# Kernel tuning notes

Measured on AMD Instinct MI355X. Metric: run time of the kernel, lower is better.

The kernel has to match this reference:

```python
import jax, jax.numpy as jnp
import numpy as np

N_NODES = 100000
EPS = 1e-5


def gcn_conv(x, src, dst, W, b):
    # PyG GCNConv: h = W x; out_i = sum_{j->i} norm_ij * h_j  (with self-loops)
    h = x @ W  # [N, out]
    deg = jax.ops.segment_sum(jnp.ones_like(src, dtype=h.dtype), dst,
                              num_segments=N_NODES) + 1.0  # +1 self-loop
    dinv = jax.lax.rsqrt(deg)  # [N]
    norm = dinv[src] * dinv[dst]  # [E]
    msgs = h[src] * norm[:, None]  # [E, out]
    agg = jax.ops.segment_sum(msgs, dst, num_segments=N_NODES)
    agg = agg + h * (1.0 / deg)[:, None]  # self-loop term, norm = deg^-1
    return agg + b


def graph_norm(x, w, b, mean_scale):
    # PyG GraphNorm, single graph: normalize over nodes per feature
    mean = jnp.mean(x, axis=0, keepdims=True)
    xc = x - mean_scale * mean
    var = jnp.mean(xc * xc, axis=0, keepdims=True)
    return w * xc * jax.lax.rsqrt(var + EPS) + b


def layer_norm(x, w, b):
    mean = jnp.mean(x, axis=-1, keepdims=True)
    xc = x - mean
    var = jnp.mean(xc * xc, axis=-1, keepdims=True)
    return w * xc * jax.lax.rsqrt(var + EPS) + b


def setup_inputs() -> dict:
    key = jax.random.key(0)
    ks = jax.random.split(key, 8)
    in_dim, hid, emb = 128, 64, 32
    x = jax.random.normal(ks[0], (N_NODES, in_dim), dtype=jnp.float32)
    edge_index = jax.random.randint(ks[1], (2, 1600000), 0, N_NODES, dtype=jnp.int64)
    s = 0.05
    return {
        'x': x,
        'edge_index': edge_index,
        'W1': jax.random.normal(ks[2], (in_dim, hid), jnp.float32) * s,
        'b1': jnp.zeros((hid,), jnp.float32),
        'W2': jax.random.normal(ks[3], (hid, hid), jnp.float32) * s,
        'b2': jnp.zeros((hid,), jnp.float32),
        'gn_w': jnp.ones((hid,), jnp.float32),
        'gn_b': jnp.zeros((hid,), jnp.float32),
        'gn_ms': jnp.ones((hid,), jnp.float32),
        'ln_w': jnp.ones((hid,), jnp.float32),
        'ln_b': jnp.zeros((hid,), jnp.float32),
        'fc_W': jax.random.normal(ks[4], (hid, emb), jnp.float32) * s,
        'fc_b': jnp.zeros((emb,), jnp.float32),
    }


def reference(x, edge_index, W1, b1, W2, b2, gn_w, gn_b, gn_ms, ln_w, ln_b, fc_W, fc_b):
    src, dst = edge_index[0], edge_index[1]
    h = jax.nn.relu(gcn_conv(x, src, dst, W1, b1))
    h = graph_norm(h, gn_w, gn_b, gn_ms)
    h = layer_norm(h, ln_w, ln_b)
    # dropout: identity in eval mode
    h = jax.nn.relu(gcn_conv(h, src, dst, W2, b2))
    h = graph_norm(h, gn_w, gn_b, gn_ms)
    h = layer_norm(h, ln_w, ln_b)
    pooled = jnp.max(h, axis=0)  # [hid]
    embedding = pooled @ fc_W + fc_b  # [emb]; emb != 1 so no sigmoid
    return embedding
```

## Files before the change

### kernel.cpp

```cpp
#include <hip/hip_runtime.h>
#include <hip/hip_bf16.h>

#define EPSV 1e-5f
#define CHUNK 256
#define CAP 6144
#define MAXNB 512
#define EPB 4096

typedef __attribute__((ext_vector_type(8))) short bf16x8;
typedef __attribute__((ext_vector_type(4))) float f32x4;

__device__ __forceinline__ ushort f2bf(float f) {
    union { float f; unsigned u; } c; c.f = f;
    unsigned u = c.u;
    return (ushort)((u + 0x7fffu + ((u >> 16) & 1u)) >> 16);
}
__device__ __forceinline__ float bf2f(ushort h) {
    union { unsigned u; float f; } c; c.u = ((unsigned)h) << 16;
    return c.f;
}
__device__ __forceinline__ float bflo(unsigned u) {
    union { unsigned u; float f; } c; c.u = u << 16;
    return c.f;
}
__device__ __forceinline__ float bfhi(unsigned u) {
    union { unsigned u; float f; } c; c.u = u & 0xFFFF0000u;
    return c.f;
}
__device__ __forceinline__ void acc8(float* a, uint4 u) {
    a[0] += bflo(u.x); a[1] += bfhi(u.x);
    a[2] += bflo(u.y); a[3] += bfhi(u.y);
    a[4] += bflo(u.z); a[5] += bfhi(u.z);
    a[6] += bflo(u.w); a[7] += bfhi(u.w);
}


__global__ void prep_kernel(const float* __restrict__ W1, const float* __restrict__ W2,
                            ushort* __restrict__ wsw1, ushort* __restrict__ wsw2,
                            uint4* __restrict__ zr, int nz16) {
    int t = blockIdx.x * blockDim.x + threadIdx.x;
    if (t < 128 * 64) {
        int k = t >> 6, n = t & 63;
        wsw1[((k >> 3) * 64 + n) * 8 + (k & 7)] = f2bf(W1[t]);
    }
    if (t < 64 * 64) {
        int k = t >> 6, n = t & 63;
        wsw2[((k >> 3) * 64 + n) * 8 + (k & 7)] = f2bf(W2[t]);
    }
    if (t < nz16) zr[t] = make_uint4(0u, 0u, 0u, 0u);
}


__global__ void __launch_bounds__(256) bucket_scatter(const int* __restrict__ ei,
                                                      int* __restrict__ bcur,
                                                      unsigned* __restrict__ bdata, int E,
                                                      int NB) {
    __shared__ int h[MAXNB];
    __shared__ int cur[MAXNB];
    int t = threadIdx.x;
    int base = blockIdx.x * EPB;
    int end = min(base + EPB, E);
    for (int b = t; b < NB; b += 256) h[b] = 0;
    __syncthreads();
    for (int e = base + t * 4; e < end; e += 1024) {
        int4 d4 = *reinterpret_cast<const int4*>(&ei[E + e]);
        atomicAdd(&h[d4.x >> 8], 1);
        atomicAdd(&h[d4.y >> 8], 1);
        atomicAdd(&h[d4.z >> 8], 1);
        atomicAdd(&h[d4.w >> 8], 1);
    }
    __syncthreads();
    for (int b = t; b < NB; b += 256) {
        int c = h[b];
        cur[b] = c ? (atomicAdd(&bcur[b], c) + b * CAP) : 0;
    }
    __syncthreads();
    for (int e = base + t * 4; e < end; e += 1024) {
        int4 s4 = *reinterpret_cast<const int4*>(&ei[e]);
        int4 d4 = *reinterpret_cast<const int4*>(&ei[E + e]);
        int p0 = atomicAdd(&cur[d4.x >> 8], 1);
        bdata[p0] = (unsigned)s4.x | ((unsigned)(d4.x & 255) << 20);
        int p1 = atomicAdd(&cur[d4.y >> 8], 1);
        bdata[p1] = (unsigned)s4.y | ((unsigned)(d4.y & 255) << 20);
        int p2 = atomicAdd(&cur[d4.z >> 8], 1);
        bdata[p2] = (unsigned)s4.z | ((unsigned)(d4.z & 255) << 20);
        int p3 = atomicAdd(&cur[d4.w >> 8], 1);
        bdata[p3] = (unsigned)s4.w | ((unsigned)(d4.w & 255) << 20);
    }
}


__global__ void __launch_bounds__(256) bucket_finish(const unsigned* __restrict__ bdata,
                                                     const int* __restrict__ bcur,
                                                     int2* __restrict__ NI,
                                                     float* __restrict__ dinv,
                                                     int* __restrict__ srcs, int N) {
    __shared__ int h[CHUNK];
    __shared__ int cur[CHUNK];
    int t = threadIdx.x;
    int beg = blockIdx.x * CAP;
    int end = beg + bcur[blockIdx.x];
    h[t] = 0;
    __syncthreads();
    for (int e = beg + t; e < end; e += 256) atomicAdd(&h[bdata[e] >> 20], 1);
    __syncthreads();
    int deg = h[t];
    int pc = (deg + 3) & ~3;
    cur[t] = pc;
    __syncthreads();
    for (int off = 1; off < 256; off <<= 1) {
        int x = (t >= off) ? cur[t - off] : 0;
        __syncthreads();
        cur[t] += x;
        __syncthreads();
    }
    int begp = beg + cur[t] - pc;
    int node = blockIdx.x * CHUNK + t;
    if (node < N) {
        NI[node] = make_int2(begp, pc);
        dinv[node] = rsqrtf((float)deg + 1.0f);
    }
    h[t] = begp;
    __syncthreads();
    for (int e = beg + t; e < end; e += 256) {
        unsigned p = bdata[e];
        int pos = atomicAdd(&h[p >> 20], 1);
        srcs[pos] = (int)((p & 0xFFFFFu) << 3);
    }
    __syncthreads();
    int zr = N * 8;
    for (int k = h[t]; k < begp + pc; k++) srcs[k] = zr;
}


__global__ void __launch_bounds__(256) mm1_kernel(const float* __restrict__ X,
                                                  const ushort* __restrict__ wsw,
                                                  const float* __restrict__ dinv,
                                                  ushort* __restrict__ Ht, int N) {
    const int KO = 4;
    int w = threadIdx.x >> 6, lane = threadIdx.x & 63;
    int m = lane & 15, q = lane >> 4;
    int row = blockIdx.x * 64 + w * 16 + m;

    bf16x8 afrag[KO];
#pragma unroll
    for (int kk = 0; kk < KO; kk++) {
        float xv[8];
        if (row < N) {
            const float4* xp = reinterpret_cast<const float4*>(X + (size_t)row * 128 + kk * 32 + q * 8);
            float4 v0 = xp[0], v1 = xp[1];
            xv[0] = v0.x; xv[1] = v0.y; xv[2] = v0.z; xv[3] = v0.w;
            xv[4] = v1.x; xv[5] = v1.y; xv[6] = v1.z; xv[7] = v1.w;
        } else {
#pragma unroll
            for (int j = 0; j < 8; j++) xv[j] = 0.f;
        }
#pragma unroll
        for (int j = 0; j < 8; j++) afrag[kk][j] = (short)f2bf(xv[j]);
    }

    float dv[4];
#pragma unroll
    for (int reg = 0; reg < 4; reg++) {
        int r = blockIdx.x * 64 + w * 16 + q * 4 + reg;
        dv[reg] = (r < N) ? dinv[r] : 0.f;
    }

    const bf16x8* wp = reinterpret_cast<const bf16x8*>(wsw);
#pragma unroll
    for (int ct = 0; ct < 4; ct++) {
        f32x4 acc = {0.f, 0.f, 0.f, 0.f};
#pragma unroll
        for (int kk = 0; kk < KO; kk++) {
            bf16x8 b = wp[(kk * 4 + q) * 64 + ct * 16 + m];
            acc = __builtin_amdgcn_mfma_f32_16x16x32_bf16(afrag[kk], b, acc, 0, 0, 0);
        }
#pragma unroll
        for (int reg = 0; reg < 4; reg++) {
            int r = blockIdx.x * 64 + w * 16 + q * 4 + reg;
            if (r < N) Ht[(size_t)r * 64 + ct * 16 + m] = f2bf(acc[reg] * dv[reg]);
        }
    }
}


__global__ void __launch_bounds__(256) mm2_kernel(
    const ushort* __restrict__ A2, const ushort* __restrict__ wsw,
    const float* __restrict__ sums, const float* __restrict__ gn_w,
    const float* __restrict__ gn_b, const float* __restrict__ gn_ms,
    const float* __restrict__ ln_w, const float* __restrict__ ln_b,
    const float* __restrict__ dinv, ushort* __restrict__ Ht, int N) {
    __shared__ float sg[64], tg[64], lwv[64], lbv[64];
    int t = threadIdx.x;
    if (t < 64) {
        float invN = 1.0f / (float)N;
        float mean = sums[t] * invN;
        float m2 = sums[64 + t] * invN;
        float ms = gn_ms[t];
        float var = m2 - 2.f * ms * mean * mean + ms * ms * mean * mean;
        float s = gn_w[t] * rsqrtf(var + EPSV);
        sg[t] = s;
        tg[t] = gn_b[t] - s * ms * mean;
        lwv[t] = ln_w[t];
        lbv[t] = ln_b[t];
    }
    __syncthreads();

    int w = t >> 6, lane = t & 63;
    int m = lane & 15, q = lane >> 4;
    int row = blockIdx.x * 64 + w * 16 + m;

    float g[16];
#pragma unroll
    for (int kk = 0; kk < 2; kk++) {
        uint4 u = make_uint4(0, 0, 0, 0);
        if (row < N)
            u = *reinterpret_cast<const uint4*>(A2 + (size_t)row * 64 + kk * 32 + q * 8);
        unsigned uu[4] = {u.x, u.y, u.z, u.w};
#pragma unroll
        for (int p = 0; p < 4; p++) {
            int f0 = kk * 32 + q * 8 + 2 * p;
            g[kk * 8 + 2 * p] = sg[f0] * bflo(uu[p]) + tg[f0];
            g[kk * 8 + 2 * p + 1] = sg[f0 + 1] * bfhi(uu[p]) + tg[f0 + 1];
        }
    }
    float s1 = 0.f;
#pragma unroll
    for (int i = 0; i < 16; i++) s1 += g[i];
    s1 += __shfl_xor(s1, 16);
    s1 += __shfl_xor(s1, 32);
    float mu = s1 * (1.f / 64.f);
    float s2 = 0.f;
#pragma unroll
    for (int i = 0; i < 16; i++) {
        float c = g[i] - mu;
        s2 += c * c;
    }
    s2 += __shfl_xor(s2, 16);
    s2 += __shfl_xor(s2, 32);
    float rs = rsqrtf(s2 * (1.f / 64.f) + EPSV);

    bf16x8 afrag[2];
#pragma unroll
    for (int kk = 0; kk < 2; kk++) {
#pragma unroll
        for (int j = 0; j < 8; j++) {
            int f = kk * 32 + q * 8 + j;
            float y = lwv[f] * (g[kk * 8 + j] - mu) * rs + lbv[f];
            afrag[kk][j] = (short)f2bf(y);
        }
    }

    float dv[4];
#pragma unroll
    for (int reg = 0; reg < 4; reg++) {
        int r = blockIdx.x * 64 + w * 16 + q * 4 + reg;
        dv[reg] = (r < N) ? dinv[r] : 0.f;
    }

    const bf16x8* wp = reinterpret_cast<const bf16x8*>(wsw);
#pragma unroll
    for (int ct = 0; ct < 4; ct++) {
        f32x4 acc = {0.f, 0.f, 0.f, 0.f};
#pragma unroll
        for (int kk = 0; kk < 2; kk++) {
            bf16x8 b = wp[(kk * 4 + q) * 64 + ct * 16 + m];
            acc = __builtin_amdgcn_mfma_f32_16x16x32_bf16(afrag[kk], b, acc, 0, 0, 0);
        }
#pragma unroll
        for (int reg = 0; reg < 4; reg++) {
            int r = blockIdx.x * 64 + w * 16 + q * 4 + reg;
            if (r < N) Ht[(size_t)r * 64 + ct * 16 + m] = f2bf(acc[reg] * dv[reg]);
        }
    }
}


__global__ void __launch_bounds__(256) agg_kernel(
    const ushort* __restrict__ Ht, const int2* __restrict__ NI, const int* __restrict__ srcs,
    const float* __restrict__ dinv, const float* __restrict__ bias,
    ushort* __restrict__ out, float* __restrict__ sums, int N) {
    int t = threadIdx.x;
    int lane = t & 63;
    int g = lane >> 3, fq = lane & 7;
    int wid = (blockIdx.x * blockDim.x + t) >> 6;
    int nw = (gridDim.x * blockDim.x) >> 6;
    const uint4* H4 = reinterpret_cast<const uint4*>(Ht);
    uint4* O4 = reinterpret_cast<uint4*>(out);
    const int ZR = N * 8;
    float bb[8];
#pragma unroll
    for (int j = 0; j < 8; j++) bb[j] = bias[fq * 8 + j];
    float ps1[8] = {0, 0, 0, 0, 0, 0, 0, 0}, ps2[8] = {0, 0, 0, 0, 0, 0, 0, 0};

    for (int jo = wid; jo * 8 < N; jo += nw) {
        int node = jo * 8 + g;
        bool valid = node < N;
        int2 info = valid ? NI[node] : make_int2(0, 0);
        float di = valid ? dinv[node] : 0.f;
        int e = info.x, end = info.x + info.y;
        float a[8] = {0, 0, 0, 0, 0, 0, 0, 0};
        for (; e + 8 <= end; e += 8) {
            int4 i0 = *reinterpret_cast<const int4*>(&srcs[e]);
            int4 i1 = *reinterpret_cast<const int4*>(&srcs[e + 4]);
            uint4 u0 = H4[i0.x + fq];
            uint4 u1 = H4[i0.y + fq];
            uint4 u2 = H4[i0.z + fq];
            uint4 u3 = H4[i0.w + fq];
            uint4 u4 = H4[i1.x + fq];
            uint4 u5 = H4[i1.y + fq];
            uint4 u6 = H4[i1.z + fq];
            uint4 u7 = H4[i1.w + fq];
            acc8(a, u0); acc8(a, u1); acc8(a, u2); acc8(a, u3);
            acc8(a, u4); acc8(a, u5); acc8(a, u6); acc8(a, u7);
        }
        if (e < end) {
            int4 i0 = *reinterpret_cast<const int4*>(&srcs[e]);
            uint4 u0 = H4[i0.x + fq];
            uint4 u1 = H4[i0.y + fq];
            uint4 u2 = H4[i0.z + fq];
            uint4 u3 = H4[i0.w + fq];
            acc8(a, u0); acc8(a, u1); acc8(a, u2); acc8(a, u3);
        }
        uint4 us = H4[(valid ? node * 8 : ZR) + fq];
        float sf[8] = {bflo(us.x), bfhi(us.x), bflo(us.y), bfhi(us.y),
                       bflo(us.z), bfhi(us.z), bflo(us.w), bfhi(us.w)};
        float vv[8];
#pragma unroll
        for (int j = 0; j < 8; j++) vv[j] = fmaxf(di * a[j] + di * sf[j] + bb[j], 0.f);
        if (valid) {
            uint4 o;
            o.x = (unsigned)f2bf(vv[0]) | ((unsigned)f2bf(vv[1]) << 16);
            o.y = (unsigned)f2bf(vv[2]) | ((unsigned)f2bf(vv[3]) << 16);
            o.z = (unsigned)f2bf(vv[4]) | ((unsigned)f2bf(vv[5]) << 16);
            o.w = (unsigned)f2bf(vv[6]) | ((unsigned)f2bf(vv[7]) << 16);
            O4[(size_t)node * 8 + fq] = o;
#pragma unroll
            for (int j = 0; j < 8; j++) {
                ps1[j] += vv[j];
                ps2[j] += vv[j] * vv[j];
            }
        }
    }

    __shared__ float red[4][128];
    int wv = t >> 6;
#pragma unroll
    for (int j = 0; j < 8; j++) {
        float s = ps1[j], q = ps2[j];
        s += __shfl_xor(s, 8); s += __shfl_xor(s, 16); s += __shfl_xor(s, 32);
        q += __shfl_xor(q, 8); q += __shfl_xor(q, 16); q += __shfl_xor(q, 32);
        if (g == 0) {
            red[wv][fq * 8 + j] = s;
            red[wv][64 + fq * 8 + j] = q;
        }
    }
    __syncthreads();
    if (t < 128) {
        float v = red[0][t] + red[1][t] + red[2][t] + red[3][t];
        atomicAdd(&sums[t], v);
    }
}


__device__ __forceinline__ unsigned fkey(float f) {
    unsigned u = __float_as_uint(f);
    return (u & 0x80000000u) ? ~u : (u | 0x80000000u);
}

__global__ void __launch_bounds__(256) gnlnmax_final(
    const ushort* __restrict__ A, const float* __restrict__ sums,
    const float* __restrict__ gn_w, const float* __restrict__ gn_b,
    const float* __restrict__ gn_ms, const float* __restrict__ ln_w,
    const float* __restrict__ ln_b, unsigned* __restrict__ pooled,
    unsigned* __restrict__ done, const float* __restrict__ fc_W,
    const float* __restrict__ fc_b, float* __restrict__ out, int N) {
    __shared__ float sg[64], tg[64];
    int t = threadIdx.x;
    if (t < 64) {
        float invN = 1.0f / (float)N;
        float mean = sums[t] * invN;
        float m2 = sums[64 + t] * invN;
        float ms = gn_ms[t];
        float var = m2 - 2.f * ms * mean * mean + ms * ms * mean * mean;
        float s = gn_w[t] * rsqrtf(var + EPSV);
        sg[t] = s;
        tg[t] = gn_b[t] - s * ms * mean;
    }
    __syncthreads();

    int lane = t & 63;
    int g = lane >> 3, fq = lane & 7;
    float sgv[8], tgv[8], lwv[8], lbv[8];
#pragma unroll
    for (int j = 0; j < 8; j++) {
        sgv[j] = sg[fq * 8 + j];
        tgv[j] = tg[fq * 8 + j];
        lwv[j] = ln_w[fq * 8 + j];
        lbv[j] = ln_b[fq * 8 + j];
    }

    int wid = (blockIdx.x * blockDim.x + t) >> 6;
    int nw = (gridDim.x * blockDim.x) >> 6;
    const uint4* A4 = reinterpret_cast<const uint4*>(A);
    float mx[8];
#pragma unroll
    for (int j = 0; j < 8; j++) mx[j] = -3.4e38f;

    for (int jo = wid; jo * 8 < N; jo += nw) {
        int row = jo * 8 + g;
        bool valid = row < N;
        uint4 u = A4[(size_t)(valid ? row : 0) * 8 + fq];
        float y[8];
        y[0] = sgv[0] * bflo(u.x) + tgv[0];
        y[1] = sgv[1] * bfhi(u.x) + tgv[1];
        y[2] = sgv[2] * bflo(u.y) + tgv[2];
        y[3] = sgv[3] * bfhi(u.y) + tgv[3];
        y[4] = sgv[4] * bflo(u.z) + tgv[4];
        y[5] = sgv[5] * bfhi(u.z) + tgv[5];
        y[6] = sgv[6] * bflo(u.w) + tgv[6];
        y[7] = sgv[7] * bfhi(u.w) + tgv[7];
        float s1 = 0.f;
#pragma unroll
        for (int j = 0; j < 8; j++) s1 += y[j];
        s1 += __shfl_xor(s1, 1);
        s1 += __shfl_xor(s1, 2);
        s1 += __shfl_xor(s1, 4);
        float mu = s1 * (1.f / 64.f);
        float s2 = 0.f;
#pragma unroll
        for (int j = 0; j < 8; j++) {
            float c = y[j] - mu;
            s2 += c * c;
        }
        s2 += __shfl_xor(s2, 1);
        s2 += __shfl_xor(s2, 2);
        s2 += __shfl_xor(s2, 4);
        float rs = rsqrtf(s2 * (1.f / 64.f) + EPSV);
        if (valid) {
#pragma unroll
            for (int j = 0; j < 8; j++)
                mx[j] = fmaxf(mx[j], lwv[j] * (y[j] - mu) * rs + lbv[j]);
        }
    }

    __shared__ float red[4][64];
    int wv = t >> 6;
#pragma unroll
    for (int j = 0; j < 8; j++) {
        float m = mx[j];
        m = fmaxf(m, __shfl_xor(m, 8));
        m = fmaxf(m, __shfl_xor(m, 16));
        m = fmaxf(m, __shfl_xor(m, 32));
        if (g == 0) red[wv][fq * 8 + j] = m;
    }
    __syncthreads();
    if (t < 64) {
        float m = fmaxf(fmaxf(red[0][t], red[1][t]), fmaxf(red[2][t], red[3][t]));
        atomicMax(&pooled[t], fkey(m));
    }
    __syncthreads();
    __shared__ int islast;
    if (t == 0) {
        __threadfence();
        unsigned old = atomicAdd(done, 1u);
        islast = (old == gridDim.x - 1);
    }
    __syncthreads();
    if (islast) {
        __shared__ float p[64];
        if (t < 64) {
            __threadfence();
            unsigned u = atomicAdd(&pooled[t], 0u);
            p[t] = (u & 0x80000000u) ? __uint_as_float(u ^ 0x80000000u) : __uint_as_float(~u);
        }
        __syncthreads();
        if (t < 32) {
            float acc = fc_b[t];
#pragma unroll
            for (int f = 0; f < 64; f++) acc += p[f] * fc_W[f * 32 + t];
            out[t] = acc;
        }
    }
}


static inline size_t align_up(size_t v, size_t a) { return (v + a - 1) & ~(a - 1); }

extern "C" void kernel_launch(void* const* d_in, const int* in_sizes, int n_in, void* d_out,
                              int out_size, void* d_ws, size_t ws_size, hipStream_t stream) {
    const float* x = (const float*)d_in[0];
    const int* ei = (const int*)d_in[1];
    const float* W1 = (const float*)d_in[2];
    const float* b1 = (const float*)d_in[3];
    const float* W2 = (const float*)d_in[4];
    const float* b2 = (const float*)d_in[5];
    const float* gn_w = (const float*)d_in[6];
    const float* gn_b = (const float*)d_in[7];
    const float* gn_ms = (const float*)d_in[8];
    const float* ln_w = (const float*)d_in[9];
    const float* ln_b = (const float*)d_in[10];
    const float* fc_W = (const float*)d_in[11];
    const float* fc_b = (const float*)d_in[12];
    float* out = (float*)d_out;

    const int N = in_sizes[0] / 128;
    const int E = in_sizes[1] / 2;
    const int NB = (N + CHUNK - 1) / CHUNK;

    char* ws = (char*)d_ws;
    size_t off = 0;
    auto alloc = [&](size_t bytes) {
        char* p = ws + off;
        off = align_up(off + bytes, 256);
        return p;
    };
    int2* NI = (int2*)alloc((size_t)N * 8);
    float* dinv = (float*)alloc((size_t)N * 4);
    unsigned* bdata = (unsigned*)alloc((size_t)NB * CAP * 4);
    int* srcs = (int*)alloc((size_t)NB * CAP * 4);
    ushort* bufB = (ushort*)alloc((size_t)N * 64 * 2);
    ushort* wsw1 = (ushort*)alloc(128 * 64 * 2);
    ushort* wsw2 = (ushort*)alloc(64 * 64 * 2);
    ushort* bufA = (ushort*)alloc((size_t)N * 64 * 2);
    size_t zoff = off;
    ushort* zrow = (ushort*)alloc(128);
    float* sums = (float*)alloc(256 * 4);
    unsigned* pooled = (unsigned*)alloc(64 * 4);
    int* bcur = (int*)alloc((size_t)(NB + 1) * 4);
    unsigned* done = (unsigned*)alloc(4);
    size_t zlen = off - zoff;
    (void)zrow;

    int nbB = (E + EPB - 1) / EPB;
    prep_kernel<<<48, 256, 0, stream>>>(W1, W2, wsw1, wsw2, (uint4*)(ws + zoff),
                                        (int)(zlen / 16));
    bucket_scatter<<<nbB, 256, 0, stream>>>(ei, bcur, bdata, E, NB);
    bucket_finish<<<NB, 256, 0, stream>>>(bdata, bcur, NI, dinv, srcs, N);

    int nbMM = (N + 63) / 64;
    int nbAgg = 782;

    mm1_kernel<<<nbMM, 256, 0, stream>>>(x, wsw1, dinv, bufA, N);
    agg_kernel<<<nbAgg, 256, 0, stream>>>(bufA, NI, srcs, dinv, b1, bufB, sums, N);

    mm2_kernel<<<nbMM, 256, 0, stream>>>(bufB, wsw2, sums, gn_w, gn_b, gn_ms, ln_w, ln_b, dinv,
                                         bufA, N);
    agg_kernel<<<nbAgg, 256, 0, stream>>>(bufA, NI, srcs, dinv, b2, bufB, sums + 128, N);
    gnlnmax_final<<<512, 256, 0, stream>>>(bufB, sums + 128, gn_w, gn_b, gn_ms, ln_w, ln_b,
                                           pooled, done, fc_W, fc_b, out, N);
}
```

Before: 283.1 us.

## Quantize transformed node features to int8 with per-row scales for aggregation

The matmul kernels now write the dinv-scaled features as int8 with one float scale per row, in place of bf16. The aggregation kernel gathers 8-byte int8 groups plus a scale per neighbour and dequantizes while accumulating. This halves the bytes of the random gathers that dominate the edge aggregation, at the cost of an extra scale load per edge and reduced precision, which may exceed the reference tolerance.

```diff
diff --git a/kernel.cpp b/kernel.cpp
--- a/kernel.cpp
+++ b/kernel.cpp
@@ -27,17 +27,22 @@
     union { unsigned u; float f; } c; c.u = u & 0xFFFF0000u;
     return c.f;
 }
-__device__ __forceinline__ void acc8(float* a, uint4 u) {
-    a[0] += bflo(u.x); a[1] += bfhi(u.x);
-    a[2] += bflo(u.y); a[3] += bfhi(u.y);
-    a[4] += bflo(u.z); a[5] += bfhi(u.z);
-    a[6] += bflo(u.w); a[7] += bfhi(u.w);
+__device__ __forceinline__ void accq(float* a, uint2 g, float sc) {
+    a[0] += sc * (float)(signed char)(g.x & 0xFF);
+    a[1] += sc * (float)(signed char)((g.x >> 8) & 0xFF);
+    a[2] += sc * (float)(signed char)((g.x >> 16) & 0xFF);
+    a[3] += sc * (float)(signed char)(g.x >> 24);
+    a[4] += sc * (float)(signed char)(g.y & 0xFF);
+    a[5] += sc * (float)(signed char)((g.y >> 8) & 0xFF);
+    a[6] += sc * (float)(signed char)((g.y >> 16) & 0xFF);
+    a[7] += sc * (float)(signed char)(g.y >> 24);
 }
 
 
 __global__ void prep_kernel(const float* __restrict__ W1, const float* __restrict__ W2,
                             ushort* __restrict__ wsw1, ushort* __restrict__ wsw2,
-                            uint4* __restrict__ zr, int nz16) {
+                            uint4* __restrict__ zr, int nz16, char* __restrict__ T8,
+                            float* __restrict__ scales, int N) {
     int t = blockIdx.x * blockDim.x + threadIdx.x;
     if (t < 128 * 64) {
         int k = t >> 6, n = t & 63;
@@ -48,6 +53,8 @@
         wsw2[((k >> 3) * 64 + n) * 8 + (k & 7)] = f2bf(W2[t]);
     }
     if (t < nz16) zr[t] = make_uint4(0u, 0u, 0u, 0u);
+    if (t < 4) reinterpret_cast<uint4*>(T8 + (size_t)N * 64)[t] = make_uint4(0u, 0u, 0u, 0u);
+    if (t == 4) scales[N] = 0.f;
 }
 
 
@@ -133,14 +140,42 @@
 }
 
 
+__device__ __forceinline__ void quant_store(const f32x4* accs, const float* dv, int rbase,
+                                            int ml, char* __restrict__ T8,
+                                            float* __restrict__ scales, int N) {
+#pragma unroll
+    for (int reg = 0; reg < 4; reg++) {
+        float mx = fmaxf(fmaxf(fabsf(accs[0][reg]), fabsf(accs[1][reg])),
+                         fmaxf(fabsf(accs[2][reg]), fabsf(accs[3][reg])));
+        mx = fmaxf(mx, __shfl_xor(mx, 1));
+        mx = fmaxf(mx, __shfl_xor(mx, 2));
+        mx = fmaxf(mx, __shfl_xor(mx, 4));
+        mx = fmaxf(mx, __shfl_xor(mx, 8));
+        mx = fmaxf(mx * dv[reg], 1e-20f);
+        float inv = 127.f / mx;
+        int r = rbase + reg;
+        if (r < N) {
+            float s = dv[reg] * inv;
+#pragma unroll
+            for (int ct = 0; ct < 4; ct++) {
+                int qv = __float2int_rn(accs[ct][reg] * s);
+                T8[(size_t)r * 64 + ct * 16 + ml] = (char)qv;
+            }
+            if (ml == 0) scales[r] = mx * (1.f / 127.f);
+        }
+    }
+}
+
+
 __global__ void __launch_bounds__(256) mm1_kernel(const float* __restrict__ X,
                                                   const ushort* __restrict__ wsw,
                                                   const float* __restrict__ dinv,
-                                                  ushort* __restrict__ Ht, int N) {
+                                                  char* __restrict__ T8,
+                                                  float* __restrict__ scales, int N) {
     const int KO = 4;
     int w = threadIdx.x >> 6, lane = threadIdx.x & 63;
-    int m = lane & 15, q = lane >> 4;
-    int row = blockIdx.x * 64 + w * 16 + m;
+    int ml = lane & 15, q = lane >> 4;
+    int row = blockIdx.x * 64 + w * 16 + ml;
 
     bf16x8 afrag[KO];
 #pragma unroll
@@ -159,28 +194,27 @@
         for (int j = 0; j < 8; j++) afrag[kk][j] = (short)f2bf(xv[j]);
     }
 
+    int rbase = blockIdx.x * 64 + w * 16 + q * 4;
     float dv[4];
 #pragma unroll
     for (int reg = 0; reg < 4; reg++) {
-        int r = blockIdx.x * 64 + w * 16 + q * 4 + reg;
+        int r = rbase + reg;
         dv[reg] = (r < N) ? dinv[r] : 0.f;
     }
 
     const bf16x8* wp = reinterpret_cast<const bf16x8*>(wsw);
+    f32x4 accs[4];
 #pragma unroll
     for (int ct = 0; ct < 4; ct++) {
         f32x4 acc = {0.f, 0.f, 0.f, 0.f};
 #pragma unroll
         for (int kk = 0; kk < KO; kk++) {
-            bf16x8 b = wp[(kk * 4 + q) * 64 + ct * 16 + m];
+            bf16x8 b = wp[(kk * 4 + q) * 64 + ct * 16 + ml];
             acc = __builtin_amdgcn_mfma_f32_16x16x32_bf16(afrag[kk], b, acc, 0, 0, 0);
         }
-#pragma unroll
-        for (int reg = 0; reg < 4; reg++) {
-            int r = blockIdx.x * 64 + w * 16 + q * 4 + reg;
-            if (r < N) Ht[(size_t)r * 64 + ct * 16 + m] = f2bf(acc[reg] * dv[reg]);
-        }
-    }
+        accs[ct] = acc;
+    }
+    quant_store(accs, dv, rbase, ml, T8, scales, N);
 }
 
 
@@ -189,7 +223,8 @@
     const float* __restrict__ sums, const float* __restrict__ gn_w,
     const float* __restrict__ gn_b, const float* __restrict__ gn_ms,
     const float* __restrict__ ln_w, const float* __restrict__ ln_b,
-    const float* __restrict__ dinv, ushort* __restrict__ Ht, int N) {
+    const float* __restrict__ dinv, char* __restrict__ T8,
+    float* __restrict__ scales, int N) {
     __shared__ float sg[64], tg[64], lwv[64], lbv[64];
     int t = threadIdx.x;
     if (t < 64) {
@@ -207,8 +242,8 @@
     __syncthreads();
 
     int w = t >> 6, lane = t & 63;
-    int m = lane & 15, q = lane >> 4;
-    int row = blockIdx.x * 64 + w * 16 + m;
+    int ml = lane & 15, q = lane >> 4;
+    int row = blockIdx.x * 64 + w * 16 + ml;
 
     float g[16];
 #pragma unroll
@@ -251,33 +286,33 @@
         }
     }
 
+    int rbase = blockIdx.x * 64 + w * 16 + q * 4;
     float dv[4];
 #pragma unroll
     for (int reg = 0; reg < 4; reg++) {
-        int r = blockIdx.x * 64 + w * 16 + q * 4 + reg;
+        int r = rbase + reg;
         dv[reg] = (r < N) ? dinv[r] : 0.f;
     }
 
     const bf16x8* wp = reinterpret_cast<const bf16x8*>(wsw);
+    f32x4 accs[4];
 #pragma unroll
     for (int ct = 0; ct < 4; ct++) {
         f32x4 acc = {0.f, 0.f, 0.f, 0.f};
 #pragma unroll
         for (int kk = 0; kk < 2; kk++) {
-            bf16x8 b = wp[(kk * 4 + q) * 64 + ct * 16 + m];
+            bf16x8 b = wp[(kk * 4 + q) * 64 + ct * 16 + ml];
             acc = __builtin_amdgcn_mfma_f32_16x16x32_bf16(afrag[kk], b, acc, 0, 0, 0);
         }
-#pragma unroll
-        for (int reg = 0; reg < 4; reg++) {
-            int r = blockIdx.x * 64 + w * 16 + q * 4 + reg;
-            if (r < N) Ht[(size_t)r * 64 + ct * 16 + m] = f2bf(acc[reg] * dv[reg]);
-        }
-    }
+        accs[ct] = acc;
+    }
+    quant_store(accs, dv, rbase, ml, T8, scales, N);
 }
 
 
 __global__ void __launch_bounds__(256) agg_kernel(
-    const ushort* __restrict__ Ht, const int2* __restrict__ NI, const int* __restrict__ srcs,
+    const char* __restrict__ T8, const float* __restrict__ scales,
+    const int2* __restrict__ NI, const int* __restrict__ srcs,
     const float* __restrict__ dinv, const float* __restrict__ bias,
     ushort* __restrict__ out, float* __restrict__ sums, int N) {
     int t = threadIdx.x;
@@ -285,7 +320,7 @@
     int g = lane >> 3, fq = lane & 7;
     int wid = (blockIdx.x * blockDim.x + t) >> 6;
     int nw = (gridDim.x * blockDim.x) >> 6;
-    const uint4* H4 = reinterpret_cast<const uint4*>(Ht);
+    const uint2* H2 = reinterpret_cast<const uint2*>(T8);
     uint4* O4 = reinterpret_cast<uint4*>(out);
     const int ZR = N * 8;
     float bb[8];
@@ -303,31 +338,43 @@
         for (; e + 8 <= end; e += 8) {
             int4 i0 = *reinterpret_cast<const int4*>(&srcs[e]);
             int4 i1 = *reinterpret_cast<const int4*>(&srcs[e + 4]);
-            uint4 u0 = H4[i0.x + fq];
-            uint4 u1 = H4[i0.y + fq];
-            uint4 u2 = H4[i0.z + fq];
-            uint4 u3 = H4[i0.w + fq];
-            uint4 u4 = H4[i1.x + fq];
-            uint4 u5 = H4[i1.y + fq];
-            uint4 u6 = H4[i1.z + fq];
-            uint4 u7 = H4[i1.w + fq];
-            acc8(a, u0); acc8(a, u1); acc8(a, u2); acc8(a, u3);
-            acc8(a, u4); acc8(a, u5); acc8(a, u6); acc8(a, u7);
+            uint2 g0 = H2[i0.x + fq];
+            uint2 g1 = H2[i0.y + fq];
+            uint2 g2 = H2[i0.z + fq];
+            uint2 g3 = H2[i0.w + fq];
+            uint2 g4 = H2[i1.x + fq];
+            uint2 g5 = H2[i1.y + fq];
+            uint2 g6 = H2[i1.z + fq];
+            uint2 g7 = H2[i1.w + fq];
+            float s0 = scales[i0.x >> 3];
+            float s1 = scales[i0.y >> 3];
+            float s2 = scales[i0.z >> 3];
+            float s3 = scales[i0.w >> 3];
+            float s4 = scales[i1.x >> 3];
+            float s5 = scales[i1.y >> 3];
+            float s6 = scales[i1.z >> 3];
+            float s7 = scales[i1.w >> 3];
+            accq(a, g0, s0); accq(a, g1, s1); accq(a, g2, s2); accq(a, g3, s3);
+            accq(a, g4, s4); accq(a, g5, s5); accq(a, g6, s6); accq(a, g7, s7);
         }
         if (e < end) {
             int4 i0 = *reinterpret_cast<const int4*>(&srcs[e]);
-            uint4 u0 = H4[i0.x + fq];
-            uint4 u1 = H4[i0.y + fq];
-            uint4 u2 = H4[i0.z + fq];
-            uint4 u3 = H4[i0.w + fq];
-            acc8(a, u0); acc8(a, u1); acc8(a, u2); acc8(a, u3);
-        }
-        uint4 us = H4[(valid ? node * 8 : ZR) + fq];
-        float sf[8] = {bflo(us.x), bfhi(us.x), bflo(us.y), bfhi(us.y),
-                       bflo(us.z), bfhi(us.z), bflo(us.w), bfhi(us.w)};
+            uint2 g0 = H2[i0.x + fq];
+            uint2 g1 = H2[i0.y + fq];
+            uint2 g2 = H2[i0.z + fq];
+            uint2 g3 = H2[i0.w + fq];
+            float s0 = scales[i0.x >> 3];
+            float s1 = scales[i0.y >> 3];
+            float s2 = scales[i0.z >> 3];
+            float s3 = scales[i0.w >> 3];
+            accq(a, g0, s0); accq(a, g1, s1); accq(a, g2, s2); accq(a, g3, s3);
+        }
+        uint2 us = H2[(valid ? node * 8 : ZR) + fq];
+        float scs = scales[valid ? node : N];
+        accq(a, us, scs);
         float vv[8];
 #pragma unroll
-        for (int j = 0; j < 8; j++) vv[j] = fmaxf(di * a[j] + di * sf[j] + bb[j], 0.f);
+        for (int j = 0; j < 8; j++) vv[j] = fmaxf(di * a[j] + bb[j], 0.f);
         if (valid) {
             uint4 o;
             o.x = (unsigned)f2bf(vv[0]) | ((unsigned)f2bf(vv[1]) << 16);
@@ -522,31 +569,30 @@
     ushort* bufB = (ushort*)alloc((size_t)N * 64 * 2);
     ushort* wsw1 = (ushort*)alloc(128 * 64 * 2);
     ushort* wsw2 = (ushort*)alloc(64 * 64 * 2);
-    ushort* bufA = (ushort*)alloc((size_t)N * 64 * 2);
+    char* T8 = (char*)alloc((size_t)N * 64 + 64);
+    float* scales = (float*)alloc((size_t)(N + 1) * 4);
     size_t zoff = off;
-    ushort* zrow = (ushort*)alloc(128);
     float* sums = (float*)alloc(256 * 4);
     unsigned* pooled = (unsigned*)alloc(64 * 4);
     int* bcur = (int*)alloc((size_t)(NB + 1) * 4);
     unsigned* done = (unsigned*)alloc(4);
     size_t zlen = off - zoff;
-    (void)zrow;
 
     int nbB = (E + EPB - 1) / EPB;
     prep_kernel<<<48, 256, 0, stream>>>(W1, W2, wsw1, wsw2, (uint4*)(ws + zoff),
-                                        (int)(zlen / 16));
+                                        (int)(zlen / 16), T8, scales, N);
     bucket_scatter<<<nbB, 256, 0, stream>>>(ei, bcur, bdata, E, NB);
     bucket_finish<<<NB, 256, 0, stream>>>(bdata, bcur, NI, dinv, srcs, N);
 
     int nbMM = (N + 63) / 64;
     int nbAgg = 782;
 
-    mm1_kernel<<<nbMM, 256, 0, stream>>>(x, wsw1, dinv, bufA, N);
-    agg_kernel<<<nbAgg, 256, 0, stream>>>(bufA, NI, srcs, dinv, b1, bufB, sums, N);
+    mm1_kernel<<<nbMM, 256, 0, stream>>>(x, wsw1, dinv, T8, scales, N);
+    agg_kernel<<<nbAgg, 256, 0, stream>>>(T8, scales, NI, srcs, dinv, b1, bufB, sums, N);
 
     mm2_kernel<<<nbMM, 256, 0, stream>>>(bufB, wsw2, sums, gn_w, gn_b, gn_ms, ln_w, ln_b, dinv,
-                                         bufA, N);
-    agg_kernel<<<nbAgg, 256, 0, stream>>>(bufA, NI, srcs, dinv, b2, bufB, sums + 128, N);
+                                         T8, scales, N);
+    agg_kernel<<<nbAgg, 256, 0, stream>>>(T8, scales, NI, srcs, dinv, b2, bufB, sums + 128, N);
     gnlnmax_final<<<512, 256, 0, stream>>>(bufB, sums + 128, gn_w, gn_b, gn_ms, ln_w, ln_b,
                                            pooled, done, fc_W, fc_b, out, N);
 }
```

Result: no change. 284.0 us (+0.3%).
